# Optimization experiments

Measured on AMD Instinct MI355X. Metric: run time of the kernel, lower is better.

The kernel has to match this reference:

```python
import jax, jax.numpy as jnp
import numpy as np

D = 256      # d_model
H = 8        # nhead
HD = D // H  # head_dim
B = 16       # ragged batch size
L = 4096     # tokens per sample (equal lengths here; code handles general ragged)
NQ = 100     # instance queries per sample


def _xavier(key, shape):
    a = float(np.sqrt(6.0 / (shape[0] + shape[1])))
    return jax.random.uniform(key, shape, jnp.float32, -a, a)


def setup_inputs() -> dict:
    key = jax.random.key(0)
    ks = jax.random.split(key, 8)
    total = B * L
    source = jax.random.normal(ks[0], (total, D), jnp.float32)
    query = jax.random.normal(ks[1], (B, NQ, D), jnp.float32)
    batch_offsets = (jnp.arange(B + 1) * L).astype(jnp.int32)
    # nn.MultiheadAttention params: in-proj (split into q/k/v) + out-proj.
    Wq = _xavier(ks[2], (D, D)); bq = jnp.zeros((D,), jnp.float32)
    Wk = _xavier(ks[3], (D, D)); bk = jnp.zeros((D,), jnp.float32)
    Wv = _xavier(ks[4], (D, D)); bv = jnp.zeros((D,), jnp.float32)
    Wo = _xavier(ks[5], (D, D)); bo = jnp.zeros((D,), jnp.float32)
    return {"source": source, "query": query, "batch_offsets": batch_offsets,
            "Wq": Wq, "bq": bq, "Wk": Wk, "bk": bk, "Wv": Wv, "bv": bv,
            "Wo": Wo, "bo": bo}


def reference(source, query, batch_offsets, Wq, bq, Wk, bk, Wv, bv, Wo, bo):
    # Ragged -> padded gather (indices are concrete, computed with numpy).
    offs = np.asarray(batch_offsets)
    lens = offs[1:] - offs[:-1]                      # (B,)
    Lmax = int(lens.max())
    pos = np.arange(Lmax)
    mask = pos[None, :] < lens[:, None]              # (B, Lmax) valid keys
    idx = np.where(mask, offs[:-1, None] + pos[None, :], 0)
    kv_in = source[jnp.asarray(idx)]                 # (B, Lmax, D)

    # Projections (torch Linear: x @ W.T + b), split into heads.
    q = (query @ Wq.T + bq).reshape(B, NQ, H, HD)
    k = (kv_in @ Wk.T + bk).reshape(B, Lmax, H, HD)
    v = (kv_in @ Wv.T + bv).reshape(B, Lmax, H, HD)

    scale = 1.0 / jnp.sqrt(jnp.asarray(HD, q.dtype))
    scores = jnp.einsum("bqhd,bkhd->bhqk", q * scale, k)
    scores = jnp.where(jnp.asarray(mask)[:, None, None, :], scores, -1e30)
    attn = jax.nn.softmax(scores, axis=-1)           # (B, H, NQ, Lmax)
    ctx = jnp.einsum("bhqk,bkhd->bqhd", attn, v).reshape(B, NQ, D)
    out = ctx @ Wo.T + bo
    # Original code: dropout/norm results are discarded; residual add of query.
    return out + query
```

## Files before the change

kernel.cpp:

```cpp
#include <hip/hip_runtime.h>
#include <hip/hip_bf16.h>
#include <math.h>

#define DM     256
#define NHEAD  8
#define HDIM   32
#define QPAD   112
#define NCHUNK 8
#define BM     128
#define BN     128
#define BK     32

typedef __attribute__((ext_vector_type(8))) short bf16x8;
typedef __attribute__((ext_vector_type(4))) short bf16x4;
typedef __attribute__((ext_vector_type(4))) float f32x4;

__device__ __forceinline__ short f2bf(float f) {
  union { float f; unsigned u; } x; x.f = f;
  unsigned u = (x.u + 0x7fffu + ((x.u >> 16) & 1u)) >> 16;
  return (short)u;
}
__device__ __forceinline__ float bf2f(short s) {
  union { unsigned u; float f; } x; x.u = ((unsigned)(unsigned short)s) << 16;
  return x.f;
}
__device__ __forceinline__ bf16x8 bzero8() {
  bf16x8 v;
#pragma unroll
  for (int j = 0; j < 8; j++) v[j] = (short)0;
  return v;
}
__device__ __forceinline__ void gl2lds16(const void* g, void* l) {
  __builtin_amdgcn_global_load_lds(
      (const __attribute__((address_space(1))) unsigned*)g,
      (__attribute__((address_space(3))) unsigned*)l, 16, 0, 0);
}
__device__ __forceinline__ bf16x8 cvt8(const float* p) {
  float4 x0 = *(const float4*)p, x1 = *(const float4*)(p + 4);
  bf16x8 v;
  v[0] = f2bf(x0.x); v[1] = f2bf(x0.y); v[2] = f2bf(x0.z); v[3] = f2bf(x0.w);
  v[4] = f2bf(x1.x); v[5] = f2bf(x1.y); v[6] = f2bf(x1.z); v[7] = f2bf(x1.w);
  return v;
}

__global__ __launch_bounds__(256) void wconv_kernel(
    const float* __restrict__ Wk, const float* __restrict__ Wv,
    short* __restrict__ Wkv) {
  int idx = blockIdx.x * 256 + threadIdx.x;
  int e0 = idx * 8;
  const float* p = (e0 < DM * DM) ? (Wk + e0) : (Wv + (e0 - DM * DM));
  *(bf16x8*)(Wkv + e0) = cvt8(p);
}

__global__ __launch_bounds__(256) void q_proj_kernel(
    const float* __restrict__ query, const float* __restrict__ Wq,
    const float* __restrict__ bq, short* __restrict__ Qw, int Bn, int NQ) {
  int b  = blockIdx.x / (QPAD / 8);
  int r0 = (blockIdx.x % (QPAD / 8)) * 8;
  __shared__ __align__(16) float ql[8 * DM];
  int tid = threadIdx.x;
  for (int i = tid; i < 8 * DM; i += 256) {
    int r = r0 + (i >> 8);
    ql[i] = (r < NQ) ? query[((size_t)b * NQ + r) * DM + (i & 255)] : 0.f;
  }
  __syncthreads();
  int d = tid;
  float bias = bq[d];
  float acc[8];
#pragma unroll
  for (int qi = 0; qi < 8; qi++) acc[qi] = bias;
  const float* wrow = Wq + (size_t)d * DM;
  for (int k = 0; k < DM; k += 4) {
    float4 w = *(const float4*)(wrow + k);
#pragma unroll
    for (int qi = 0; qi < 8; qi++) {
      float4 x = *(const float4*)&ql[qi * DM + k];
      acc[qi] += x.x * w.x + x.y * w.y + x.z * w.z + x.w * w.w;
    }
  }
  const float scale = 0.17677669529663687f;
  int h = d >> 5, hd = d & 31;
#pragma unroll
  for (int qi = 0; qi < 8; qi++) {
    int r = r0 + qi;
    float v = (r < NQ) ? acc[qi] * scale : 0.f;
    Qw[(((size_t)b * NHEAD + h) * QPAD + r) * HDIM + hd] = f2bf(v);
  }
}

__global__ __launch_bounds__(256) void kv_gemm_kernel(
    const float* __restrict__ src, const short* __restrict__ Wkv,
    const float* __restrict__ bk, const float* __restrict__ bv,
    const int* __restrict__ offs, short* __restrict__ Kw,
    short* __restrict__ Vw, int T, int Bn, int Mtiles) {
  int ntile = blockIdx.x / Mtiles;
  int mtile = blockIdx.x % Mtiles;
  int t0 = mtile * BM;
  int n0 = ntile * BN;
  bool isK = (n0 < DM);
  int n0rel = n0 & (DM - 1);
  const float* bias = isK ? bk : bv;

  int tid = threadIdx.x;
  int wave = tid >> 6, lane = tid & 63;
  int l15 = lane & 15, quad = lane >> 4;
  int wm = wave >> 1, wn = wave & 1;

  __shared__ __align__(16) short As[BM][BK + 8];
  __shared__ __align__(16) short Bs[BN * BK];

  f32x4 acc[4][4];
#pragma unroll
  for (int i = 0; i < 4; i++)
#pragma unroll
    for (int j = 0; j < 4; j++) acc[i][j] = (f32x4){0.f, 0.f, 0.f, 0.f};

  for (int kk = 0; kk < DM; kk += BK) {
    __syncthreads();
#pragma unroll
    for (int s2 = 0; s2 < 2; s2++) {
      int s = tid + s2 * 256;
      int row = s >> 2, ch = s & 3;
      int tok = t0 + row;
      if (tok >= T) tok = T - 1;
      *(bf16x8*)&As[row][ch * 8] = cvt8(src + (size_t)tok * DM + kk + ch * 8);
    }
    {
      int cloc = lane >> 2;
#pragma unroll
      for (int j = 0; j < 2; j++) {
        int cb = wave * 32 + j * 16;
        int c = cb + cloc;
        int slot = (lane & 3) ^ ((c >> 1) & 3);
        const short* g = Wkv + (size_t)(n0 + c) * DM + kk + slot * 8;
        gl2lds16(g, &Bs[cb * BK]);
      }
    }
    __syncthreads();
    bf16x8 af[4], bf_[4];
#pragma unroll
    for (int mt = 0; mt < 4; mt++)
      af[mt] = *(const bf16x8*)&As[wm * 64 + mt * 16 + l15][quad * 8];
#pragma unroll
    for (int nt = 0; nt < 4; nt++) {
      int c = wn * 64 + nt * 16 + l15;
      int slot = quad ^ ((c >> 1) & 3);
      bf_[nt] = *(const bf16x8*)&Bs[c * BK + slot * 8];
    }
    if (isK) {
#pragma unroll
      for (int mt = 0; mt < 4; mt++)
#pragma unroll
        for (int nt = 0; nt < 4; nt++)
          acc[mt][nt] = __builtin_amdgcn_mfma_f32_16x16x32_bf16(
              bf_[nt], af[mt], acc[mt][nt], 0, 0, 0);
    } else {
#pragma unroll
      for (int mt = 0; mt < 4; mt++)
#pragma unroll
        for (int nt = 0; nt < 4; nt++)
          acc[mt][nt] = __builtin_amdgcn_mfma_f32_16x16x32_bf16(
              af[mt], bf_[nt], acc[mt][nt], 0, 0, 0);
    }
  }

  if (isK) {
    float bk4[4][4];
    int hK[4], hdK[4];
#pragma unroll
    for (int nt = 0; nt < 4; nt++) {
      int nbq = n0rel + wn * 64 + nt * 16 + quad * 4;
      float4 b4 = *(const float4*)(bias + nbq);
      bk4[nt][0] = b4.x; bk4[nt][1] = b4.y; bk4[nt][2] = b4.z; bk4[nt][3] = b4.w;
      hK[nt] = nbq >> 5;
      hdK[nt] = nbq & 31;
    }
    int bcur = 0;
#pragma unroll
    for (int mt = 0; mt < 4; mt++) {
      int tok = t0 + wm * 64 + mt * 16 + l15;
      if (tok >= T) continue;
      while (bcur + 1 < Bn && offs[bcur + 1] <= tok) bcur++;
      int off = offs[bcur], len = offs[bcur + 1] - off;
      int l = tok - off;
      size_t bb = (size_t)off * DM;
#pragma unroll
      for (int nt = 0; nt < 4; nt++) {
        bf16x4 p;
#pragma unroll
        for (int r = 0; r < 4; r++) p[r] = f2bf(acc[mt][nt][r] + bk4[nt][r]);
        *(bf16x4*)&Kw[bb + (size_t)hK[nt] * len * HDIM + (size_t)l * HDIM +
                      hdK[nt]] = p;
      }
    }
  } else {
    float bV[4];
    int hV[4], hdV[4];
#pragma unroll
    for (int nt = 0; nt < 4; nt++) {
      int nb = n0rel + wn * 64 + nt * 16 + l15;
      bV[nt] = bias[nb];
      hV[nt] = nb >> 5;
      hdV[nt] = nb & 31;
    }
    int bcur = 0;
#pragma unroll
    for (int mt = 0; mt < 4; mt++) {
      int tb = t0 + wm * 64 + mt * 16 + quad * 4;
      if (tb >= T) continue;
      while (bcur + 1 < Bn && offs[bcur + 1] <= tb) bcur++;
      int off = offs[bcur], len = offs[bcur + 1] - off;
      size_t bb = (size_t)off * DM;
      bool span = (tb + 3 < offs[bcur + 1]) && (tb + 3 < T);
      if (span) {
        int l = tb - off;
#pragma unroll
        for (int nt = 0; nt < 4; nt++) {
          size_t idx =
              bb + (size_t)hV[nt] * len * HDIM + (size_t)hdV[nt] * len + l;
          bf16x4 p;
#pragma unroll
          for (int r = 0; r < 4; r++) p[r] = f2bf(acc[mt][nt][r] + bV[nt]);
          if ((idx & 3) == 0) {
            *(bf16x4*)&Vw[idx] = p;
          } else {
#pragma unroll
            for (int r = 0; r < 4; r++) Vw[idx + r] = p[r];
          }
        }
      } else {
        int bc2 = bcur;
#pragma unroll
        for (int r = 0; r < 4; r++) {
          int tok = tb + r;
          if (tok >= T) continue;
          while (bc2 + 1 < Bn && offs[bc2 + 1] <= tok) bc2++;
          int off2 = offs[bc2], len2 = offs[bc2 + 1] - off2;
          int l = tok - off2;
          size_t bb2 = (size_t)off2 * DM;
#pragma unroll
          for (int nt = 0; nt < 4; nt++)
            Vw[bb2 + (size_t)hV[nt] * len2 * HDIM + (size_t)hdV[nt] * len2 +
               l] = f2bf(acc[mt][nt][r] + bV[nt]);
        }
      }
    }
  }
}

__global__ __launch_bounds__(448) void attn_kernel(
    const short* __restrict__ Qw, const short* __restrict__ Kw,
    const short* __restrict__ Vw, const int* __restrict__ offs,
    short* __restrict__ Ops, float* __restrict__ Ml, int Bn) {
  int c  = blockIdx.x % NCHUNK;
  int bh = blockIdx.x / NCHUNK;
  int h = bh % NHEAD, b = bh / NHEAD;
  int wave = threadIdx.x >> 6, lane = threadIdx.x & 63;
  int l15 = lane & 15, quad = lane >> 4;

  int off = offs[b], len = offs[b + 1] - off;
  int cl = ((len + NCHUNK * 32 - 1) / (NCHUNK * 32)) * 32;
  int kstart = c * cl;
  int kend   = min(kstart + cl, len);

  const short* Kh = Kw + (size_t)off * DM + (size_t)h * len * HDIM;
  const short* Vh = Vw + (size_t)off * DM + (size_t)h * len * HDIM;

  int row16 = wave * 16 + l15;
  bf16x8 aq = *(const bf16x8*)(
      Qw + (((size_t)b * NHEAD + h) * QPAD + row16) * HDIM + quad * 8);

  f32x4 o[2];
#pragma unroll
  for (int j = 0; j < 2; j++) o[j] = (f32x4){0.f, 0.f, 0.f, 0.f};
  float mrun[4], lrun[4];
#pragma unroll
  for (int r = 0; r < 4; r++) { mrun[r] = -1e30f; lrun[r] = 0.f; }

  __shared__ __align__(16) short plds[7][16][40];

  for (int kb = kstart; kb < kend; kb += 32) {
    bool valid[2];
    bf16x8 bk_[2];
#pragma unroll
    for (int nt = 0; nt < 2; nt++) {
      int key = kb + nt * 16 + l15;
      valid[nt] = key < kend;
      bk_[nt] = valid[nt]
                    ? *(const bf16x8*)(Kh + (size_t)key * HDIM + quad * 8)
                    : bzero8();
    }
    f32x4 zero = {0.f, 0.f, 0.f, 0.f};
    f32x4 s[2];
#pragma unroll
    for (int nt = 0; nt < 2; nt++)
      s[nt] = __builtin_amdgcn_mfma_f32_16x16x32_bf16(aq, bk_[nt], zero, 0, 0, 0);
#pragma unroll
    for (int r = 0; r < 4; r++) {
      float v0 = valid[0] ? s[0][r] : -1e30f;
      float v1 = valid[1] ? s[1][r] : -1e30f;
      float t = fmaxf(v0, v1);
      t = fmaxf(t, __shfl_xor(t, 1, 16));
      t = fmaxf(t, __shfl_xor(t, 2, 16));
      t = fmaxf(t, __shfl_xor(t, 4, 16));
      t = fmaxf(t, __shfl_xor(t, 8, 16));
      float mn = fmaxf(mrun[r], t);
      float al = __expf(mrun[r] - mn);
      float p0 = valid[0] ? __expf(v0 - mn) : 0.f;
      float p1 = valid[1] ? __expf(v1 - mn) : 0.f;
      float rs = p0 + p1;
      rs += __shfl_xor(rs, 1, 16);
      rs += __shfl_xor(rs, 2, 16);
      rs += __shfl_xor(rs, 4, 16);
      rs += __shfl_xor(rs, 8, 16);
      lrun[r] = al * lrun[r] + rs;
      mrun[r] = mn;
      o[0][r] *= al;
      o[1][r] *= al;
      plds[wave][quad * 4 + r][l15]      = f2bf(p0);
      plds[wave][quad * 4 + r][16 + l15] = f2bf(p1);
    }
    bf16x8 pa = *(const bf16x8*)&plds[wave][l15][quad * 8];
    bf16x8 bv_[2];
#pragma unroll
    for (int ht = 0; ht < 2; ht++) {
      int hd = ht * 16 + l15;
      int k0 = kb + quad * 8;
      const short* p = Vh + (size_t)hd * len + k0;
      if (k0 + 7 < len) {
        bv_[ht] = *(const bf16x8*)p;
      } else {
        bf16x8 v;
#pragma unroll
        for (int j = 0; j < 8; j++) v[j] = (k0 + j < len) ? p[j] : (short)0;
        bv_[ht] = v;
      }
    }
#pragma unroll
    for (int ht = 0; ht < 2; ht++)
      o[ht] = __builtin_amdgcn_mfma_f32_16x16x32_bf16(pa, bv_[ht], o[ht], 0, 0, 0);
  }

#pragma unroll
  for (int r = 0; r < 4; r++) {
    int row = wave * 16 + quad * 4 + r;
    size_t base = (((size_t)c * Bn + b) * NHEAD + h) * QPAD + row;
#pragma unroll
    for (int ht = 0; ht < 2; ht++)
      Ops[base * HDIM + ht * 16 + l15] = f2bf(o[ht][r]);
    if (l15 == 0) {
      Ml[base * 2]     = mrun[r];
      Ml[base * 2 + 1] = lrun[r];
    }
  }
}

__global__ __launch_bounds__(256) void combine_kernel(
    const short* __restrict__ Ops, const float* __restrict__ Ml,
    const float* __restrict__ query, const float* __restrict__ Wo,
    const float* __restrict__ bo, float* __restrict__ out, int Bn, int NQ) {
  int bpb = (NQ + 7) / 8;
  int b  = blockIdx.x / bpb;
  int q0 = (blockIdx.x % bpb) * 8;
  __shared__ __align__(16) float ctx[8 * DM];
  int d = threadIdx.x;
  int h = d >> 5, hd = d & 31;
#pragma unroll
  for (int qi = 0; qi < 8; qi++) {
    int q = q0 + qi;
    float val = 0.f;
    if (q < NQ) {
      float mc[NCHUNK], lc[NCHUNK], M = -1e30f;
#pragma unroll
      for (int c = 0; c < NCHUNK; c++) {
        size_t base = (((size_t)c * Bn + b) * NHEAD + h) * QPAD + q;
        mc[c] = Ml[base * 2];
        lc[c] = Ml[base * 2 + 1];
        M = fmaxf(M, mc[c]);
      }
      float L = 0.f, acc = 0.f;
#pragma unroll
      for (int c = 0; c < NCHUNK; c++) {
        size_t base = (((size_t)c * Bn + b) * NHEAD + h) * QPAD + q;
        float w = __expf(mc[c] - M);
        L += lc[c] * w;
        acc += w * bf2f(Ops[base * HDIM + hd]);
      }
      val = (L > 0.f) ? acc / L : 0.f;
    }
    ctx[qi * DM + d] = val;
  }
  __syncthreads();
  const float* wrow = Wo + (size_t)d * DM;
  float acc[8];
  float bias = bo[d];
#pragma unroll
  for (int qi = 0; qi < 8; qi++) acc[qi] = bias;
  for (int k = 0; k < DM; k += 4) {
    float4 w = *(const float4*)(wrow + k);
#pragma unroll
    for (int qi = 0; qi < 8; qi++) {
      float4 x = *(const float4*)&ctx[qi * DM + k];
      acc[qi] += x.x * w.x + x.y * w.y + x.z * w.z + x.w * w.w;
    }
  }
#pragma unroll
  for (int qi = 0; qi < 8; qi++) {
    int q = q0 + qi;
    if (q < NQ)
      out[((size_t)b * NQ + q) * DM + d] =
          acc[qi] + query[((size_t)b * NQ + q) * DM + d];
  }
}

extern "C" void kernel_launch(void* const* d_in, const int* in_sizes, int n_in,
                              void* d_out, int out_size, void* d_ws,
                              size_t ws_size, hipStream_t stream) {
  const float* src   = (const float*)d_in[0];
  const float* query = (const float*)d_in[1];
  const int*   offs  = (const int*)d_in[2];
  const float* Wq = (const float*)d_in[3];
  const float* bq = (const float*)d_in[4];
  const float* Wk = (const float*)d_in[5];
  const float* bk = (const float*)d_in[6];
  const float* Wv = (const float*)d_in[7];
  const float* bv = (const float*)d_in[8];
  const float* Wo = (const float*)d_in[9];
  const float* bo = (const float*)d_in[10];
  float* out = (float*)d_out;

  int T  = in_sizes[0] / DM;
  int Bn = in_sizes[2] - 1;
  int NQ = in_sizes[1] / (Bn * DM);

  char* w = (char*)d_ws;
  size_t qsz = (size_t)Bn * NHEAD * QPAD * HDIM * 2;
  size_t ksz = (size_t)T * DM * 2;
  size_t osz = (size_t)NCHUNK * Bn * NHEAD * QPAD * HDIM * 2;
  size_t msz = (size_t)NCHUNK * Bn * NHEAD * QPAD * 2 * 4;
  short* Qw  = (short*)w;
  short* Kw  = (short*)(w + qsz);
  short* Vw  = (short*)(w + qsz + ksz);
  short* Ops = (short*)(w + qsz + 2 * ksz);
  float* Mlp = (float*)(w + qsz + 2 * ksz + osz);
  short* Wkv = (short*)(w + qsz + 2 * ksz + osz + msz);

  int Mtiles = (T + BM - 1) / BM;

  wconv_kernel<<<(2 * DM * DM) / (256 * 8), 256, 0, stream>>>(Wk, Wv, Wkv);
  q_proj_kernel<<<Bn * (QPAD / 8), 256, 0, stream>>>(query, Wq, bq, Qw, Bn, NQ);
  kv_gemm_kernel<<<Mtiles * (2 * DM / BN), 256, 0, stream>>>(
      src, Wkv, bk, bv, offs, Kw, Vw, T, Bn, Mtiles);
  attn_kernel<<<Bn * NHEAD * NCHUNK, 448, 0, stream>>>(Qw, Kw, Vw, offs, Ops,
                                                       Mlp, Bn);
  combine_kernel<<<Bn * ((NQ + 7) / 8), 256, 0, stream>>>(Ops, Mlp, query, Wo,
                                                          bo, out, Bn, NQ);
}
```

Measured before the change: 271.7 us.

## Double-buffer KV GEMM K-loop and stage V transpose through LDS

The KV projection GEMM now double-buffers its A and B tiles in shared memory. The next k-slice is prefetched into registers and LDS while the current one runs on MFMA, and A uses a swizzled layout. Block order is changed so the four N tiles of one M tile run as adjacent blocks, which improves L2 reuse of each source tile. The V epilogue transposes through an LDS tile so each store writes 8 contiguous tokens instead of scattered 4-element writes. This costs extra shared memory and a few more barriers.

```diff
diff --git a/kernel.cpp b/kernel.cpp
--- a/kernel.cpp
+++ b/kernel.cpp
@@ -10,6 +10,7 @@
 #define BM     128
 #define BN     128
 #define BK     32
+#define VTS    136
 
 typedef __attribute__((ext_vector_type(8))) short bf16x8;
 typedef __attribute__((ext_vector_type(4))) short bf16x4;
@@ -37,6 +38,12 @@
 }
 __device__ __forceinline__ bf16x8 cvt8(const float* p) {
   float4 x0 = *(const float4*)p, x1 = *(const float4*)(p + 4);
+  bf16x8 v;
+  v[0] = f2bf(x0.x); v[1] = f2bf(x0.y); v[2] = f2bf(x0.z); v[3] = f2bf(x0.w);
+  v[4] = f2bf(x1.x); v[5] = f2bf(x1.y); v[6] = f2bf(x1.z); v[7] = f2bf(x1.w);
+  return v;
+}
+__device__ __forceinline__ bf16x8 cvt8r(float4 x0, float4 x1) {
   bf16x8 v;
   v[0] = f2bf(x0.x); v[1] = f2bf(x0.y); v[2] = f2bf(x0.z); v[3] = f2bf(x0.w);
   v[4] = f2bf(x1.x); v[5] = f2bf(x1.y); v[6] = f2bf(x1.z); v[7] = f2bf(x1.w);
@@ -92,11 +99,10 @@
     const float* __restrict__ src, const short* __restrict__ Wkv,
     const float* __restrict__ bk, const float* __restrict__ bv,
     const int* __restrict__ offs, short* __restrict__ Kw,
-    short* __restrict__ Vw, int T, int Bn, int Mtiles) {
-  int ntile = blockIdx.x / Mtiles;
-  int mtile = blockIdx.x % Mtiles;
-  int t0 = mtile * BM;
-  int n0 = ntile * BN;
+    short* __restrict__ Vw, int T, int Bn) {
+  int mtile = blockIdx.x >> 2;
+  int ntile = blockIdx.x & 3;
+  int t0 = mtile * BM, n0 = ntile * BN;
   bool isK = (n0 < DM);
   int n0rel = n0 & (DM - 1);
   const float* bias = isK ? bk : bv;
@@ -106,8 +112,7 @@
   int l15 = lane & 15, quad = lane >> 4;
   int wm = wave >> 1, wn = wave & 1;
 
-  __shared__ __align__(16) short As[BM][BK + 8];
-  __shared__ __align__(16) short Bs[BN * BK];
+  __shared__ __align__(16) short smem[BN * VTS];
 
   f32x4 acc[4][4];
 #pragma unroll
@@ -115,38 +120,71 @@
 #pragma unroll
     for (int j = 0; j < 4; j++) acc[i][j] = (f32x4){0.f, 0.f, 0.f, 0.f};
 
-  for (int kk = 0; kk < DM; kk += BK) {
+  int arow = tid >> 1, ah = tid & 1;
+  int asw = (arow >> 1) & 3;
+  int ac0 = 2 * ah, ac1 = 2 * ah + 1;
+  const float* asrc =
+      src + (size_t)((t0 + arow < T) ? (t0 + arow) : (T - 1)) * DM;
+  int bco = lane >> 2, bsl = lane & 3;
+
+#pragma unroll
+  for (int j = 0; j < 2; j++) {
+    int cbase = wave * 32 + j * 16;
+    int col = cbase + bco;
+    int slot = bsl ^ ((col >> 1) & 3);
+    gl2lds16(Wkv + (size_t)(n0 + col) * DM + slot * 8,
+             smem + 8192 + cbase * BK);
+  }
+  {
+    float4 a00 = *(const float4*)(asrc + ac0 * 8);
+    float4 a01 = *(const float4*)(asrc + ac0 * 8 + 4);
+    float4 a10 = *(const float4*)(asrc + ac1 * 8);
+    float4 a11 = *(const float4*)(asrc + ac1 * 8 + 4);
+    *(bf16x8*)&smem[arow * BK + (ac0 ^ asw) * 8] = cvt8r(a00, a01);
+    *(bf16x8*)&smem[arow * BK + (ac1 ^ asw) * 8] = cvt8r(a10, a11);
+  }
+
+  int arsw[4], bcsw[4];
+#pragma unroll
+  for (int mt = 0; mt < 4; mt++) {
+    int row = wm * 64 + mt * 16 + l15;
+    arsw[mt] = row * BK + (quad ^ ((row >> 1) & 3)) * 8;
+  }
+#pragma unroll
+  for (int nt = 0; nt < 4; nt++) {
+    int col = wn * 64 + nt * 16 + l15;
+    bcsw[nt] = col * BK + (quad ^ ((col >> 1) & 3)) * 8;
+  }
+
+  for (int i = 0; i < 8; i++) {
+    int cur = i & 1, nxt = (i + 1) & 1;
+    const short* Ac = smem + cur * 4096;
+    const short* Bc = smem + 8192 + cur * 4096;
+    short* An = smem + nxt * 4096;
+    short* Bnx = smem + 8192 + nxt * 4096;
     __syncthreads();
-#pragma unroll
-    for (int s2 = 0; s2 < 2; s2++) {
-      int s = tid + s2 * 256;
-      int row = s >> 2, ch = s & 3;
-      int tok = t0 + row;
-      if (tok >= T) tok = T - 1;
-      *(bf16x8*)&As[row][ch * 8] = cvt8(src + (size_t)tok * DM + kk + ch * 8);
-    }
-    {
-      int cloc = lane >> 2;
+    float4 p00, p01, p10, p11;
+    bool pre = (i < 7);
+    if (pre) {
+      int kn = (i + 1) * BK;
 #pragma unroll
       for (int j = 0; j < 2; j++) {
-        int cb = wave * 32 + j * 16;
-        int c = cb + cloc;
-        int slot = (lane & 3) ^ ((c >> 1) & 3);
-        const short* g = Wkv + (size_t)(n0 + c) * DM + kk + slot * 8;
-        gl2lds16(g, &Bs[cb * BK]);
-      }
-    }
-    __syncthreads();
+        int cbase = wave * 32 + j * 16;
+        int col = cbase + bco;
+        int slot = bsl ^ ((col >> 1) & 3);
+        gl2lds16(Wkv + (size_t)(n0 + col) * DM + kn + slot * 8,
+                 Bnx + cbase * BK);
+      }
+      p00 = *(const float4*)(asrc + kn + ac0 * 8);
+      p01 = *(const float4*)(asrc + kn + ac0 * 8 + 4);
+      p10 = *(const float4*)(asrc + kn + ac1 * 8);
+      p11 = *(const float4*)(asrc + kn + ac1 * 8 + 4);
+    }
     bf16x8 af[4], bf_[4];
 #pragma unroll
-    for (int mt = 0; mt < 4; mt++)
-      af[mt] = *(const bf16x8*)&As[wm * 64 + mt * 16 + l15][quad * 8];
-#pragma unroll
-    for (int nt = 0; nt < 4; nt++) {
-      int c = wn * 64 + nt * 16 + l15;
-      int slot = quad ^ ((c >> 1) & 3);
-      bf_[nt] = *(const bf16x8*)&Bs[c * BK + slot * 8];
-    }
+    for (int mt = 0; mt < 4; mt++) af[mt] = *(const bf16x8*)&Ac[arsw[mt]];
+#pragma unroll
+    for (int nt = 0; nt < 4; nt++) bf_[nt] = *(const bf16x8*)&Bc[bcsw[nt]];
     if (isK) {
 #pragma unroll
       for (int mt = 0; mt < 4; mt++)
@@ -161,6 +199,10 @@
         for (int nt = 0; nt < 4; nt++)
           acc[mt][nt] = __builtin_amdgcn_mfma_f32_16x16x32_bf16(
               af[mt], bf_[nt], acc[mt][nt], 0, 0, 0);
+    }
+    if (pre) {
+      *(bf16x8*)&An[arow * BK + (ac0 ^ asw) * 8] = cvt8r(p00, p01);
+      *(bf16x8*)&An[arow * BK + (ac1 ^ asw) * 8] = cvt8r(p10, p11);
     }
   }
 
@@ -195,53 +237,48 @@
     }
   } else {
     float bV[4];
-    int hV[4], hdV[4];
-#pragma unroll
-    for (int nt = 0; nt < 4; nt++) {
-      int nb = n0rel + wn * 64 + nt * 16 + l15;
-      bV[nt] = bias[nb];
-      hV[nt] = nb >> 5;
-      hdV[nt] = nb & 31;
-    }
-    int bcur = 0;
+#pragma unroll
+    for (int nt = 0; nt < 4; nt++) bV[nt] = bias[n0rel + wn * 64 + nt * 16 + l15];
+    __syncthreads();
+    short* Vt = smem;
 #pragma unroll
     for (int mt = 0; mt < 4; mt++) {
-      int tb = t0 + wm * 64 + mt * 16 + quad * 4;
-      if (tb >= T) continue;
-      while (bcur + 1 < Bn && offs[bcur + 1] <= tb) bcur++;
-      int off = offs[bcur], len = offs[bcur + 1] - off;
-      size_t bb = (size_t)off * DM;
-      bool span = (tb + 3 < offs[bcur + 1]) && (tb + 3 < T);
-      if (span) {
-        int l = tb - off;
-#pragma unroll
-        for (int nt = 0; nt < 4; nt++) {
-          size_t idx =
-              bb + (size_t)hV[nt] * len * HDIM + (size_t)hdV[nt] * len + l;
-          bf16x4 p;
-#pragma unroll
-          for (int r = 0; r < 4; r++) p[r] = f2bf(acc[mt][nt][r] + bV[nt]);
-          if ((idx & 3) == 0) {
-            *(bf16x4*)&Vw[idx] = p;
-          } else {
-#pragma unroll
-            for (int r = 0; r < 4; r++) Vw[idx + r] = p[r];
-          }
-        }
+#pragma unroll
+      for (int nt = 0; nt < 4; nt++) {
+        int col = wn * 64 + nt * 16 + l15;
+        int tokl = wm * 64 + mt * 16 + quad * 4;
+        bf16x4 p;
+#pragma unroll
+        for (int r = 0; r < 4; r++) p[r] = f2bf(acc[mt][nt][r] + bV[nt]);
+        *(bf16x4*)&Vt[col * VTS + tokl] = p;
+      }
+    }
+    __syncthreads();
+#pragma unroll
+    for (int pp = 0; pp < 8; pp++) {
+      int col = pp * 16 + (tid >> 4);
+      int tk0 = (tid & 15) * 8;
+      bf16x8 v = *(const bf16x8*)&Vt[col * VTS + tk0];
+      int n = n0rel + col, h = n >> 5, hd = n & 31;
+      int tok = t0 + tk0;
+      if (tok >= T) continue;
+      int bcur = 0;
+      while (bcur + 1 < Bn && offs[bcur + 1] <= tok) bcur++;
+      int off = offs[bcur], end = offs[bcur + 1], len = end - off;
+      size_t idx = (size_t)off * DM + (size_t)h * len * HDIM +
+                   (size_t)hd * len + (tok - off);
+      if (tok + 7 < end && tok + 7 < T && (idx & 7) == 0) {
+        *(bf16x8*)&Vw[idx] = v;
       } else {
         int bc2 = bcur;
 #pragma unroll
-        for (int r = 0; r < 4; r++) {
-          int tok = tb + r;
-          if (tok >= T) continue;
-          while (bc2 + 1 < Bn && offs[bc2 + 1] <= tok) bc2++;
+        for (int j = 0; j < 8; j++) {
+          int tj = tok + j;
+          if (tj >= T) break;
+          while (bc2 + 1 < Bn && offs[bc2 + 1] <= tj) bc2++;
           int off2 = offs[bc2], len2 = offs[bc2 + 1] - off2;
-          int l = tok - off2;
-          size_t bb2 = (size_t)off2 * DM;
-#pragma unroll
-          for (int nt = 0; nt < 4; nt++)
-            Vw[bb2 + (size_t)hV[nt] * len2 * HDIM + (size_t)hdV[nt] * len2 +
-               l] = f2bf(acc[mt][nt][r] + bV[nt]);
+          Vw[(size_t)off2 * DM + (size_t)h * len2 * HDIM +
+             (size_t)hd * len2 + (tj - off2)] = v[j];
         }
       }
     }
@@ -449,8 +486,8 @@
 
   wconv_kernel<<<(2 * DM * DM) / (256 * 8), 256, 0, stream>>>(Wk, Wv, Wkv);
   q_proj_kernel<<<Bn * (QPAD / 8), 256, 0, stream>>>(query, Wq, bq, Qw, Bn, NQ);
-  kv_gemm_kernel<<<Mtiles * (2 * DM / BN), 256, 0, stream>>>(
-      src, Wkv, bk, bv, offs, Kw, Vw, T, Bn, Mtiles);
+  kv_gemm_kernel<<<Mtiles * 4, 256, 0, stream>>>(src, Wkv, bk, bv, offs, Kw,
+                                                 Vw, T, Bn);
   attn_kernel<<<Bn * NHEAD * NCHUNK, 448, 0, stream>>>(Qw, Kw, Vw, offs, Ops,
                                                        Mlp, Bn);
   combine_kernel<<<Bn * ((NQ + 7) / 8), 256, 0, stream>>>(Ops, Mlp, query, Wo,
```

Measured after the change: 332.1 us. 1.22x slower.
